# Performance work log

Measured on AMD Instinct MI355X. Metric: run time of the kernel, lower is better.

Reference implementation:

```python
import jax, jax.numpy as jnp
import numpy as np

STATE_LEN, SEQ_LEN, HIDDEN = 2048, 4096, 2048

def setup_inputs() -> dict:
    key = jax.random.key(0)
    k1, k2, k3, k4 = jax.random.split(key, 4)
    scale = 1.0 / np.sqrt(HIDDEN)
    return {
        "out_state": jax.random.normal(k1, (STATE_LEN, HIDDEN), dtype=jnp.float32),
        "history": jax.random.normal(k2, (SEQ_LEN, HIDDEN), dtype=jnp.float32),
        "W": jax.random.normal(k3, (HIDDEN, HIDDEN), dtype=jnp.float32) * scale,
        "b": jax.random.normal(k4, (HIDDEN,), dtype=jnp.float32) * scale,
    }

def reference(out_state, history, W, b):
    # method='general': energy_j = Linear(history_j) = history_j @ W.T + b
    # score[i, j] = out_state_i . energy_j  -> batched GEMM replacing the double loop
    energies = history @ W.T + b                 # [seq_len, hidden]
    scores = jnp.einsum('ih,jh->ij', out_state, energies)  # [state_len, seq_len]
    # F.softmax on a 2D tensor (legacy default) normalizes over dim=1 (rows)
    return jax.nn.softmax(scores, axis=-1)
```

## Files before the change

kernel.cpp:

```cpp
#include <hip/hip_runtime.h>


#define STATE_LEN 2048
#define SEQ_LEN   4096
#define HIDDEN    2048

#define BM 128
#define BK 32

typedef __bf16 bf16x8 __attribute__((ext_vector_type(8)));
typedef float f32x4 __attribute__((ext_vector_type(4)));

__device__ __forceinline__ unsigned short f32_to_bf16(float f) {
  unsigned u = __float_as_uint(f);
  u += 0x7FFFu + ((u >> 16) & 1u);
  return (unsigned short)(u >> 16);
}
__device__ __forceinline__ float bf16_to_f32(unsigned short h) {
  return __uint_as_float(((unsigned)h) << 16);
}

__device__ __forceinline__ void gld16(const void* g, void* l) {
  __builtin_amdgcn_global_load_lds(
      (const __attribute__((address_space(1))) unsigned int*)g,
      (__attribute__((address_space(3))) unsigned int*)l,
      16, 0, 0);
}

__global__ __launch_bounds__(256) void split_kernel(
    const float* __restrict__ in, unsigned short* __restrict__ hi,
    unsigned short* __restrict__ lo, int n) {
  int i = (blockIdx.x * 256 + threadIdx.x) * 4;
  if (i >= n) return;
  float4 v = *(const float4*)&in[i];
  ushort4 h, l;
  h.x = f32_to_bf16(v.x); l.x = f32_to_bf16(v.x - bf16_to_f32(h.x));
  h.y = f32_to_bf16(v.y); l.y = f32_to_bf16(v.y - bf16_to_f32(h.y));
  h.z = f32_to_bf16(v.z); l.z = f32_to_bf16(v.z - bf16_to_f32(h.z));
  h.w = f32_to_bf16(v.w); l.w = f32_to_bf16(v.w - bf16_to_f32(h.w));
  *(ushort4*)&hi[i] = h;
  *(ushort4*)&lo[i] = l;
}

__global__ __launch_bounds__(256) void transpose_split_kernel(
    const float* __restrict__ in, unsigned short* __restrict__ hi,
    unsigned short* __restrict__ lo, int rows, int cols) {
  __shared__ float tile[32][33];
  const int bx = blockIdx.x * 32;
  const int by = blockIdx.y * 32;
  const int tx = threadIdx.x;
  const int ty = threadIdx.y;
#pragma unroll
  for (int i = 0; i < 32; i += 8)
    tile[ty + i][tx] = in[(size_t)(by + ty + i) * cols + (bx + tx)];
  __syncthreads();
#pragma unroll
  for (int i = 0; i < 32; i += 8) {
    float x = tile[tx][ty + i];
    unsigned short h = f32_to_bf16(x);
    unsigned short l = f32_to_bf16(x - bf16_to_f32(h));
    size_t o = (size_t)(bx + ty + i) * rows + (by + tx);
    hi[o] = h;
    lo[o] = l;
  }
}

template <int BN, bool SPLIT_OUT>
__global__ __launch_bounds__(256, 2) void gemm_bt_split(
    const unsigned short* __restrict__ Ahi, const unsigned short* __restrict__ Alo,
    const unsigned short* __restrict__ Bhi, const unsigned short* __restrict__ Blo,
    float* __restrict__ Cf, unsigned short* __restrict__ Chi,
    unsigned short* __restrict__ Clo, int M, int N, int K) {
  constexpr int NI = BN / 32;
  __shared__ __align__(16) unsigned short sAhi[BM * BK];
  __shared__ __align__(16) unsigned short sAlo[BM * BK];
  __shared__ __align__(16) unsigned short sBhi[BN * BK];
  __shared__ __align__(16) unsigned short sBlo[BN * BK];

  const int t = threadIdx.x;
  const int tileM = blockIdx.y * BM;
  const int tileN = blockIdx.x * BN;
  const int rr = t >> 2;
  const int cc = t & 3;

  const int lane = t & 63;
  const int wave = t >> 6;
  const int wm = wave >> 1;
  const int wn = wave & 1;
  const int lr = lane & 15;
  const int kqc = lane >> 4;

  f32x4 acc[4][NI] = {};

  for (int k0 = 0; k0 < K; k0 += BK) {
#pragma unroll
    for (int it = 0; it < 2; ++it) {
      const int r = it * 64 + rr;
      const int q = cc ^ ((r >> 1) & 3);
      const size_t ga = (size_t)(tileM + r) * K + k0 + q * 8;
      const int ls = r * BK + cc * 8;
      gld16(Ahi + ga, &sAhi[ls]);
      gld16(Alo + ga, &sAlo[ls]);
    }
#pragma unroll
    for (int it = 0; it < BN / 64; ++it) {
      const int r = it * 64 + rr;
      const int q = cc ^ ((r >> 1) & 3);
      const size_t gb = (size_t)(tileN + r) * K + k0 + q * 8;
      const int ls = r * BK + cc * 8;
      gld16(Bhi + gb, &sBhi[ls]);
      gld16(Blo + gb, &sBlo[ls]);
    }
    __syncthreads();

    bf16x8 ah[4], al[4], bh[NI], bl[NI];
#pragma unroll
    for (int mi = 0; mi < 4; ++mi) {
      const int R = wm * 64 + mi * 16 + lr;
      const int off = R * BK + (kqc ^ ((R >> 1) & 3)) * 8;
      ah[mi] = *(const bf16x8*)&sAhi[off];
      al[mi] = *(const bf16x8*)&sAlo[off];
    }
#pragma unroll
    for (int ni = 0; ni < NI; ++ni) {
      const int R = wn * (BN / 2) + ni * 16 + lr;
      const int off = R * BK + (kqc ^ ((R >> 1) & 3)) * 8;
      bh[ni] = *(const bf16x8*)&sBhi[off];
      bl[ni] = *(const bf16x8*)&sBlo[off];
    }
#pragma unroll
    for (int mi = 0; mi < 4; ++mi)
#pragma unroll
      for (int ni = 0; ni < NI; ++ni) {
        acc[mi][ni] = __builtin_amdgcn_mfma_f32_16x16x32_bf16(ah[mi], bh[ni], acc[mi][ni], 0, 0, 0);
        acc[mi][ni] = __builtin_amdgcn_mfma_f32_16x16x32_bf16(ah[mi], bl[ni], acc[mi][ni], 0, 0, 0);
        acc[mi][ni] = __builtin_amdgcn_mfma_f32_16x16x32_bf16(al[mi], bh[ni], acc[mi][ni], 0, 0, 0);
      }
    __syncthreads();
  }

#pragma unroll
  for (int mi = 0; mi < 4; ++mi)
#pragma unroll
    for (int ni = 0; ni < NI; ++ni)
#pragma unroll
      for (int e = 0; e < 4; ++e) {
        const int row = tileM + wm * 64 + mi * 16 + (lane >> 4) * 4 + e;
        const int col = tileN + wn * (BN / 2) + ni * 16 + lr;
        const float x = acc[mi][ni][e];
        const size_t o = (size_t)row * N + col;
        if (SPLIT_OUT) {
          const unsigned short h = f32_to_bf16(x);
          Chi[o] = h;
          Clo[o] = f32_to_bf16(x - bf16_to_f32(h));
        } else {
          Cf[o] = x;
        }
      }
}

__global__ __launch_bounds__(256) void softmax_rows(float* __restrict__ d, int cols) {
  const int row = blockIdx.x;
  float* p = d + (size_t)row * cols;
  const int t = threadIdx.x;
  const int lane = t & 63;
  const int wave = t >> 6;
  __shared__ float sred[4];

  float4 v[4];
  float m = -3.0e38f;
#pragma unroll
  for (int k = 0; k < 4; ++k) {
    v[k] = *(float4*)&p[(t + k * 256) * 4];
    m = fmaxf(m, fmaxf(fmaxf(v[k].x, v[k].y), fmaxf(v[k].z, v[k].w)));
  }
#pragma unroll
  for (int off = 32; off > 0; off >>= 1) m = fmaxf(m, __shfl_xor(m, off, 64));
  if (lane == 0) sred[wave] = m;
  __syncthreads();
  m = fmaxf(fmaxf(sred[0], sred[1]), fmaxf(sred[2], sred[3]));
  __syncthreads();

  float s = 0.f;
#pragma unroll
  for (int k = 0; k < 4; ++k) {
    v[k].x = __expf(v[k].x - m);
    v[k].y = __expf(v[k].y - m);
    v[k].z = __expf(v[k].z - m);
    v[k].w = __expf(v[k].w - m);
    s += (v[k].x + v[k].y) + (v[k].z + v[k].w);
  }
#pragma unroll
  for (int off = 32; off > 0; off >>= 1) s += __shfl_xor(s, off, 64);
  if (lane == 0) sred[wave] = s;
  __syncthreads();
  s = (sred[0] + sred[1]) + (sred[2] + sred[3]);
  const float inv = 1.0f / s;
#pragma unroll
  for (int k = 0; k < 4; ++k) {
    v[k].x *= inv; v[k].y *= inv; v[k].z *= inv; v[k].w *= inv;
    *(float4*)&p[(t + k * 256) * 4] = v[k];
  }
}

extern "C" void kernel_launch(void* const* d_in, const int* in_sizes, int n_in,
                              void* d_out, int out_size, void* d_ws, size_t ws_size,
                              hipStream_t stream) {
  const float* out_state = (const float*)d_in[0];
  const float* history   = (const float*)d_in[1];
  const float* W         = (const float*)d_in[2];
  float* out = (float*)d_out;

  char* ws = (char*)d_ws;
  const size_t MB = 1ull << 20;
  unsigned short* ohi  = (unsigned short*)(ws + 0 * MB);
  unsigned short* olo  = (unsigned short*)(ws + 8 * MB);
  unsigned short* wthi = (unsigned short*)(ws + 16 * MB);
  unsigned short* wtlo = (unsigned short*)(ws + 24 * MB);
  unsigned short* hhi  = (unsigned short*)(ws + 32 * MB);
  unsigned short* hlo  = (unsigned short*)(ws + 48 * MB);
  unsigned short* thi  = (unsigned short*)(ws + 64 * MB);
  unsigned short* tlo  = (unsigned short*)(ws + 72 * MB);

  split_kernel<<<(STATE_LEN * HIDDEN) / 1024, 256, 0, stream>>>(out_state, ohi, olo,
                                                                STATE_LEN * HIDDEN);
  transpose_split_kernel<<<dim3(HIDDEN / 32, HIDDEN / 32), dim3(32, 8), 0, stream>>>(
      W, wthi, wtlo, HIDDEN, HIDDEN);
  split_kernel<<<(SEQ_LEN * HIDDEN) / 1024, 256, 0, stream>>>(history, hhi, hlo,
                                                              SEQ_LEN * HIDDEN);
  gemm_bt_split<64, true><<<dim3(HIDDEN / 64, STATE_LEN / BM), 256, 0, stream>>>(
      ohi, olo, wthi, wtlo, nullptr, thi, tlo, STATE_LEN, HIDDEN, HIDDEN);
  gemm_bt_split<128, false><<<dim3(SEQ_LEN / 128, STATE_LEN / BM), 256, 0, stream>>>(
      thi, tlo, hhi, hlo, out, nullptr, nullptr, STATE_LEN, SEQ_LEN, HIDDEN);
  softmax_rows<<<STATE_LEN, 256, 0, stream>>>(out, SEQ_LEN);
}
```

Measured before the change: 292.1 us.

## Split-K the first GEMM with 128-wide tiles and add reduce-split kernel

The out_state·W^T GEMM now uses 128x128 tiles with a two-way K split, which gives 512 blocks instead of the earlier 512 blocks of 128x64. It writes fp32 partial sums to workspace, and a new kernel adds the two partials and splits the sum into bf16 hi/lo. The aim is better data reuse per block from the larger tiles while keeping the number of blocks for occupancy. The cost is an extra 32MB fp32 write and read plus one more kernel launch. The thi/tlo buffers now reuse the workspace slots that held the transposed W.

```diff
diff --git a/kernel.cpp b/kernel.cpp
--- a/kernel.cpp
+++ b/kernel.cpp
@@ -65,7 +65,24 @@
   }
 }
 
-template <int BN, bool SPLIT_OUT>
+__global__ __launch_bounds__(256) void reduce_split(
+    const float* __restrict__ p0, const float* __restrict__ p1,
+    unsigned short* __restrict__ hi, unsigned short* __restrict__ lo, int n) {
+  int i = (blockIdx.x * 256 + threadIdx.x) * 4;
+  if (i >= n) return;
+  float4 a = *(const float4*)&p0[i];
+  float4 b = *(const float4*)&p1[i];
+  a.x += b.x; a.y += b.y; a.z += b.z; a.w += b.w;
+  ushort4 h, l;
+  h.x = f32_to_bf16(a.x); l.x = f32_to_bf16(a.x - bf16_to_f32(h.x));
+  h.y = f32_to_bf16(a.y); l.y = f32_to_bf16(a.y - bf16_to_f32(h.y));
+  h.z = f32_to_bf16(a.z); l.z = f32_to_bf16(a.z - bf16_to_f32(h.z));
+  h.w = f32_to_bf16(a.w); l.w = f32_to_bf16(a.w - bf16_to_f32(h.w));
+  *(ushort4*)&hi[i] = h;
+  *(ushort4*)&lo[i] = l;
+}
+
+template <int BN, bool SPLIT_OUT, int KSPLIT>
 __global__ __launch_bounds__(256, 2) void gemm_bt_split(
     const unsigned short* __restrict__ Ahi, const unsigned short* __restrict__ Alo,
     const unsigned short* __restrict__ Bhi, const unsigned short* __restrict__ Blo,
@@ -80,6 +97,9 @@
   const int t = threadIdx.x;
   const int tileM = blockIdx.y * BM;
   const int tileN = blockIdx.x * BN;
+  const int kBase = (KSPLIT > 1) ? blockIdx.z * (K / KSPLIT) : 0;
+  const int kEnd = kBase + K / KSPLIT;
+  if (KSPLIT > 1) Cf += (size_t)blockIdx.z * M * N;
   const int rr = t >> 2;
   const int cc = t & 3;
 
@@ -92,7 +112,7 @@
 
   f32x4 acc[4][NI] = {};
 
-  for (int k0 = 0; k0 < K; k0 += BK) {
+  for (int k0 = kBase; k0 < kEnd; k0 += BK) {
 #pragma unroll
     for (int it = 0; it < 2; ++it) {
       const int r = it * 64 + rr;
@@ -219,8 +239,9 @@
   unsigned short* wtlo = (unsigned short*)(ws + 24 * MB);
   unsigned short* hhi  = (unsigned short*)(ws + 32 * MB);
   unsigned short* hlo  = (unsigned short*)(ws + 48 * MB);
-  unsigned short* thi  = (unsigned short*)(ws + 64 * MB);
-  unsigned short* tlo  = (unsigned short*)(ws + 72 * MB);
+  float*          part = (float*)(ws + 64 * MB);
+  unsigned short* thi  = (unsigned short*)(ws + 16 * MB);
+  unsigned short* tlo  = (unsigned short*)(ws + 24 * MB);
 
   split_kernel<<<(STATE_LEN * HIDDEN) / 1024, 256, 0, stream>>>(out_state, ohi, olo,
                                                                 STATE_LEN * HIDDEN);
@@ -228,9 +249,13 @@
       W, wthi, wtlo, HIDDEN, HIDDEN);
   split_kernel<<<(SEQ_LEN * HIDDEN) / 1024, 256, 0, stream>>>(history, hhi, hlo,
                                                               SEQ_LEN * HIDDEN);
-  gemm_bt_split<64, true><<<dim3(HIDDEN / 64, STATE_LEN / BM), 256, 0, stream>>>(
-      ohi, olo, wthi, wtlo, nullptr, thi, tlo, STATE_LEN, HIDDEN, HIDDEN);
-  gemm_bt_split<128, false><<<dim3(SEQ_LEN / 128, STATE_LEN / BM), 256, 0, stream>>>(
-      thi, tlo, hhi, hlo, out, nullptr, nullptr, STATE_LEN, SEQ_LEN, HIDDEN);
+  gemm_bt_split<128, false, 2>
+      <<<dim3(HIDDEN / 128, STATE_LEN / 128, 2), 256, 0, stream>>>(
+          ohi, olo, wthi, wtlo, part, nullptr, nullptr, STATE_LEN, HIDDEN, HIDDEN);
+  reduce_split<<<(STATE_LEN * HIDDEN) / 1024, 256, 0, stream>>>(
+      part, part + (size_t)STATE_LEN * HIDDEN, thi, tlo, STATE_LEN * HIDDEN);
+  gemm_bt_split<128, false, 1>
+      <<<dim3(SEQ_LEN / 128, STATE_LEN / 128), 256, 0, stream>>>(
+          thi, tlo, hhi, hlo, out, nullptr, nullptr, STATE_LEN, SEQ_LEN, HIDDEN);
   softmax_rows<<<STATE_LEN, 256, 0, stream>>>(out, SEQ_LEN);
 }
```

Result: faster. 280.7 us (-3.9%).
